# Optimization experiments

Measured on AMD Instinct MI355X. Metric: run time of the kernel, lower is better.

The kernel has to match this reference:

```python
import jax, jax.numpy as jnp
import numpy as np
from functools import partial

EPS = 1e-6
SINKHORN_ITERS = 10

def sinkhorn(logits):
    # log-space Sinkhorn normalization -> doubly-stochastic soft permutation
    M = logits
    for _ in range(SINKHORN_ITERS):
        M = M - jax.scipy.special.logsumexp(M, axis=1, keepdims=True)
        M = M - jax.scipy.special.logsumexp(M, axis=0, keepdims=True)
    return jnp.exp(M)

def r_poly(a):
    delta = 0.5 - a
    num = 0.25 + 1.65811 * delta + 2.15388 * delta**2 + 8.2844 * delta**3 + 6.16764 * delta**4
    den = a * (1.0 - a)
    den = jnp.where(jnp.abs(den) < EPS, EPS, den)
    return num / den

def power_r(x, y, ra, w0, w1):
    ra = jnp.where(jnp.abs(ra) < EPS, EPS, ra)
    return (w0 * x**ra + w1 * y**ra) ** (1.0 / ra)

def F_upper(x, y, a, w0, w1):
    # generalized combine for a in [0.5, 2); x,y pre-clamped to [EPS, 1-EPS]
    xy = x * y
    mn = jnp.minimum(x, y)
    lin = w0 * x + w1 * y
    p = jnp.sqrt(jnp.maximum(3.0 / jnp.maximum(2.0 - a, EPS) - 1.0, EPS))
    r1 = xy ** p                                      # 1.25 < a < 2
    r3 = 4.0 * ((1.25 - a) * mn + (a - 1.0) * xy)     # 1 < a < 1.25
    ra = r_poly(jnp.clip(a, 0.75, 1.0 - EPS))
    r5 = power_r(x, y, ra, w0, w1)                    # 0.75 <= a < 1
    R = r_poly(jnp.float32(0.75))
    r6 = (3.0 - 4.0 * a) * lin + (4.0 * a - 2.0) * power_r(x, y, R, w0, w1)
    r0 = jnp.where((jnp.abs(x - 1.0) < EPS) & (jnp.abs(y - 1.0) < EPS), 1.0, 0.0)
    out = lin                                          # a ~ 0.5 / fallback
    out = jnp.where((a > 0.5) & (a < 0.75), r6, out)
    out = jnp.where((a >= 0.75) & (a < 1.0), r5, out)
    out = jnp.where(jnp.abs(a - 1.0) < EPS, mn, out)
    out = jnp.where((a > 1.0) & (a < 1.25), r3, out)
    out = jnp.where(jnp.abs(a - 1.25) < EPS, xy, out)
    out = jnp.where((a > 1.25) & (a < 2.0), r1, out)
    out = jnp.where(jnp.abs(a - 2.0) < EPS, r0, out)
    return out

def F_comb(x, y, a, w0, w1):
    x = jnp.clip(jnp.nan_to_num(x, nan=EPS), EPS, 1.0 - EPS)
    y = jnp.clip(jnp.nan_to_num(y, nan=EPS), EPS, 1.0 - EPS)
    a = jnp.clip(jnp.nan_to_num(a, nan=-1.0, posinf=2.0 - EPS, neginf=-1.0 + EPS), -1.0 + EPS, 2.0 - EPS)
    hi = F_upper(x, y, a, w0, w1)
    a_flip = jnp.clip(1.0 - a, -1.0 + EPS, 2.0 - EPS)
    lo = 1.0 - F_upper(1.0 - x, 1.0 - y, a_flip, w0, w1)  # rule 8 (single-level recursion)
    return jnp.where(a < 0.5 - EPS, lo, hi)

def combine(left, right, w, b):
    w_soft = jax.nn.softmax(w)
    a_scaled = jax.nn.sigmoid(b) * 3.0 - 1.0
    nres = F_comb(left, right, a_scaled, w_soft[0], w_soft[1])
    return jnp.where(jnp.isnan(nres), a_scaled, nres)

def setup_inputs() -> dict:
    key = jax.random.key(0)
    k1, k2, k3, k4 = jax.random.split(key, 4)
    B, L = 65536, 256
    x = jax.random.uniform(k1, (B, L), dtype=jnp.float32)
    logits = jax.random.normal(k2, (L, L), dtype=jnp.float32)
    weights = jax.random.uniform(k3, (L - 1, 2), dtype=jnp.float32) + 0.5   # uniform(0.5, 1.5)
    biases = jax.random.uniform(k4, (L - 1,), dtype=jnp.float32) * 3.0 - 1.0
    return {"x": x, "logits": logits, "weights": weights, "biases": biases}

def reference(x, logits, weights, biases):
    P = sinkhorn(logits)                  # (L, L) soft permutation
    leaf_values = x @ P                   # (B, L)
    leaves = leaf_values.T                # (L, B)
    out0 = combine(leaves[0], leaves[1], weights[0], biases[0])

    def step(carry, inp):
        leaf, w, b = inp
        out = combine(carry, leaf, w, b)
        return out, None

    final, _ = jax.lax.scan(step, out0, (leaves[2:], weights[1:], biases[1:]))
    return final[:, None]                 # (B, 1)
```

## Files before the change

kernel.cpp:

```cpp
#include <hip/hip_runtime.h>

#define EPS 1e-6f

typedef unsigned short u16;
typedef u16   u16x4  __attribute__((ext_vector_type(4)));
typedef u16   u16x8  __attribute__((ext_vector_type(8)));
typedef float f32x4  __attribute__((ext_vector_type(4)));
typedef _Float16 f16x8 __attribute__((ext_vector_type(8)));

enum { BR_LIN = 0, BR_R6, BR_R5, BR_MIN, BR_R3, BR_XY, BR_R1, BR_R0 };

__device__ __forceinline__ u16 f2h(float f) { return __builtin_bit_cast(u16, (_Float16)f); }

__device__ __forceinline__ f16x8 lds_f16x8(const u16* p) {
  u16x8 r = *(const u16x8*)p;
  return __builtin_bit_cast(f16x8, r);
}

__device__ __forceinline__ f32x4 mfma16(f16x8 a, f16x8 b, f32x4 c) {
  return __builtin_amdgcn_mfma_f32_16x16x32_f16(a, b, c, 0, 0, 0);
}

__device__ __forceinline__ float fexp2(float x) {
  float r; asm("v_exp_f32 %0, %1" : "=v"(r) : "v"(x)); return r;
}
__device__ __forceinline__ float flog2(float x) {
  float r; asm("v_log_f32 %0, %1" : "=v"(r) : "v"(x)); return r;
}

__device__ __forceinline__ float r_poly_f(float a) {
  float d  = 0.5f - a;
  float d2 = d * d;
  float num = 0.25f + 1.65811f * d + 2.15388f * d2 + 8.2844f * d2 * d + 6.16764f * d2 * d2;
  float den = a * (1.0f - a);
  if (fabsf(den) < EPS) den = EPS;
  return num / den;
}

__device__ __forceinline__ void leaf_pre(float leaf, f32x4 p0, f32x4 p2,
                                         float& Y, float& w1Y, float& w1ey, float& cply) {
  float fx = p0[0], w1 = p0[2], rs = p2[0], cp = p2[2], sx = p2[3];
  float yy = fminf(fmaxf(leaf, EPS), 1.0f - EPS);
  Y = fmaf(sx, yy, fx);
  float ly = flog2(Y);
  w1Y  = w1 * Y;
  w1ey = w1 * fexp2(rs * ly);
  cply = cp * ly;
}

__device__ __forceinline__ float step_carry(float carry, float Y, float w1Y, float w1ey, float cply,
                                            f32x4 p0, f32x4 p1, f32x4 p2) {
  float fx = p0[0], w0 = p0[1], s_lin = p0[3];
  float s_mn = p1[0], s_xy = p1[1], s_pm = p1[2], s_pow = p1[3];
  float rs = p2[0], rinv = p2[1], cp = p2[2], sx = p2[3];

  float xx = fminf(fmaxf(carry, EPS), 1.0f - EPS);
  float X  = fmaf(sx, xx, fx);
  float lx = flog2(X);
  float pw = fexp2(fmaf(cp, lx, cply));
  float ex = fexp2(rs * lx);
  float s  = fmaf(w0, ex, w1ey);
  float pm = fexp2(rinv * flog2(s));

  float r = s_lin * fmaf(w0, X, w1Y);
  r = fmaf(s_mn, fminf(X, Y), r);
  r = fmaf(s_xy, X * Y, r);
  r = fmaf(s_pm, pm, r);
  r = fmaf(s_pow, pw, r);
  return fmaf(sx, r, fx);
}

__global__ __launch_bounds__(1024, 4) void sinkhorn_kernel(
    const float* __restrict__ logits, u16* __restrict__ PTf,
    const float* __restrict__ W, const float* __restrict__ Bv,
    float* __restrict__ prm12) {
  const int t  = threadIdx.x;

  if (t < 255) {
    int i = t;
    float w0r = W[2 * i], w1r = W[2 * i + 1];
    float m  = fmaxf(w0r, w1r);
    float e0 = expf(w0r - m), e1 = expf(w1r - m);
    float inv = 1.0f / (e0 + e1);
    float w0 = e0 * inv, w1 = e1 * inv;

    float b   = Bv[i];
    float sig = 1.0f / (1.0f + expf(-b));
    float a_fb = sig * 3.0f - 1.0f;

    float a = a_fb;
    if (__builtin_isnan(a)) a = -1.0f;
    a = fminf(fmaxf(a, -1.0f + EPS), 2.0f - EPS);
    int flip = (a < 0.5f - EPS) ? 1 : 0;
    float aa = a;
    if (flip) aa = fminf(fmaxf(1.0f - a, -1.0f + EPS), 2.0f - EPS);

    int br; float c0 = 0.f, c1 = 0.f, c2 = 0.f, c3 = 0.f;
    if (fabsf(aa - 2.0f) < EPS) br = BR_R0;
    else if (aa > 1.25f && aa < 2.0f) {
      br = BR_R1;
      c0 = sqrtf(fmaxf(3.0f / fmaxf(2.0f - aa, EPS) - 1.0f, EPS));
    } else if (fabsf(aa - 1.25f) < EPS) br = BR_XY;
    else if (aa > 1.0f && aa < 1.25f) { br = BR_R3; c0 = 1.25f - aa; c1 = aa - 1.0f; }
    else if (fabsf(aa - 1.0f) < EPS) br = BR_MIN;
    else if (aa >= 0.75f && aa < 1.0f) {
      br = BR_R5;
      float ac = fminf(fmaxf(aa, 0.75f), 1.0f - EPS);
      float ra = r_poly_f(ac);
      if (fabsf(ra) < EPS) ra = EPS;
      c0 = ra; c1 = 1.0f / ra;
    } else if (aa > 0.5f && aa < 0.75f) {
      br = BR_R6;
      c0 = 3.0f - 4.0f * aa; c1 = 4.0f * aa - 2.0f;
      float R = r_poly_f(0.75f);
      if (fabsf(R) < EPS) R = EPS;
      c2 = R; c3 = 1.0f / R;
    } else br = BR_LIN;

    float s_lin = 0.f, s_mn = 0.f, s_xy = 0.f, s_pm = 0.f, s_pow = 0.f;
    float rs = 1.0f, rinv = 1.0f, cp = 0.0f;
    if (br == BR_R1)       { s_pow = 1.0f; cp = c0; }
    else if (br == BR_XY)  { s_xy = 1.0f; }
    else if (br == BR_R3)  { s_mn = 4.0f * c0; s_xy = 4.0f * c1; }
    else if (br == BR_MIN) { s_mn = 1.0f; }
    else if (br == BR_R5)  { s_pm = 1.0f; rs = c0; rinv = c1; }
    else if (br == BR_R6)  { s_lin = c0; s_pm = c1; rs = c2; rinv = c3; }
    else if (br == BR_LIN) { s_lin = 1.0f; }

    float* o12 = prm12 + i * 12;
    o12[0] = (float)flip; o12[1] = w0;  o12[2] = w1;   o12[3] = s_lin;
    o12[4] = s_mn;        o12[5] = s_xy; o12[6] = s_pm; o12[7] = s_pow;
    o12[8] = rs;          o12[9] = rinv; o12[10] = cp;  o12[11] = 1.0f - 2.0f * (float)flip;
  }

  __shared__ float alpha[256], beta[256];
  __shared__ float psum[256][33];

  const int R  = t >> 5;
  const int C  = t & 31;
  const int r0 = R << 3;

  float e[8][8];
  #pragma unroll
  for (int dr = 0; dr < 8; ++dr) {
    const float* row = logits + (r0 + dr) * 256 + C;
    #pragma unroll
    for (int m = 0; m < 8; ++m) e[dr][m] = __expf(row[m << 5]);
  }

  if (t < 256) beta[t] = 1.0f;
  __syncthreads();

  for (int it = 0; it < 10; ++it) {
    {
      float bv[8], acc[8];
      #pragma unroll
      for (int m = 0; m < 8; ++m) bv[m] = beta[C + (m << 5)];
      #pragma unroll
      for (int dr = 0; dr < 8; ++dr) {
        float s = 0.f;
        #pragma unroll
        for (int m = 0; m < 8; ++m) s += e[dr][m] * bv[m];
        acc[dr] = s;
      }
      #pragma unroll
      for (int dr = 0; dr < 8; ++dr) psum[r0 + dr][C] = acc[dr];
    }
    __syncthreads();
    if (t < 256) {
      float s = 0.f;
      #pragma unroll
      for (int j = 0; j < 32; ++j) s += psum[t][j];
      alpha[t] = 1.0f / s;
    }
    __syncthreads();
    {
      float av[8], acc[8];
      #pragma unroll
      for (int dr = 0; dr < 8; ++dr) av[dr] = alpha[r0 + dr];
      #pragma unroll
      for (int m = 0; m < 8; ++m) {
        float s = 0.f;
        #pragma unroll
        for (int dr = 0; dr < 8; ++dr) s += e[dr][m] * av[dr];
        acc[m] = s;
      }
      #pragma unroll
      for (int m = 0; m < 8; ++m) psum[C + (m << 5)][R] = acc[m];
    }
    __syncthreads();
    if (t < 256) {
      float s = 0.f;
      #pragma unroll
      for (int j = 0; j < 32; ++j) s += psum[t][j];
      beta[t] = 1.0f / s;
    }
    __syncthreads();
  }

  float av[8], bv[8];
  #pragma unroll
  for (int dr = 0; dr < 8; ++dr) av[dr] = alpha[r0 + dr];
  #pragma unroll
  for (int m = 0; m < 8; ++m) bv[m] = beta[C + (m << 5)];

  #pragma unroll
  for (int m = 0; m < 8; ++m) {
    int l = C + (m << 5);
    u16x8 vh;
    #pragma unroll
    for (int dr = 0; dr < 8; ++dr) vh[dr] = f2h(av[dr] * e[dr][m] * bv[m]);
    *(u16x8*)(PTf + l * 256 + r0) = vh;
  }
}

#define CSTR 68

__global__ __launch_bounds__(256, 4) void gemm_chain_kernel(
    const float* __restrict__ x, const u16* __restrict__ PTf,
    const float* __restrict__ prm12, float* __restrict__ out) {
  __shared__ __align__(16) char smem[32768];
  u16* xs = (u16*)smem;
  u16* pt = (u16*)(smem + 4096);
  float* qlds = (float*)(smem + 20480);
  float* cbuf = (float*)smem;

  const int t    = threadIdx.x;
  const int w    = t >> 6;
  const int lane = t & 63;
  const int bl   = lane & 15;
  const int kh   = lane >> 4;
  const int wm   = w >> 1;
  const int wn   = w & 1;
  const int b0   = blockIdx.x * 64;

  const int xrow = t >> 2;
  const int xsl  = t & 3;

  for (int j = t; j < 3060; j += 256) qlds[j] = prm12[j];

  f32x4 acc[8][2];
  #pragma unroll
  for (int m = 0; m < 8; ++m) {
    acc[m][0] = f32x4{0.f, 0.f, 0.f, 0.f};
    acc[m][1] = f32x4{0.f, 0.f, 0.f, 0.f};
  }

  f32x4 xr[2];
  u16x8 pr[4];

  #pragma unroll
  for (int j = 0; j < 2; ++j)
    xr[j] = *(const f32x4*)(x + (b0 + xrow) * 256 + ((xsl + 4 * j) << 2));
  #pragma unroll
  for (int j = 0; j < 4; ++j) {
    int c = t + 256 * j, r = c >> 2, s = c & 3, g = s ^ ((r >> 1) & 3);
    pr[j] = *(const u16x8*)(PTf + r * 256 + (g << 3));
  }

  for (int kc = 0; kc < 8; ++kc) {
    #pragma unroll
    for (int j = 0; j < 2; ++j) {
      int slot = xsl + 4 * j;
      u16x4 hv;
      #pragma unroll
      for (int e = 0; e < 4; ++e) hv[e] = f2h(xr[j][e]);
      int g = slot >> 1, sub = slot & 1;
      *(u16x4*)(xs + xrow * 32 + ((g ^ ((xrow >> 1) & 3)) << 3) + (sub << 2)) = hv;
    }
    #pragma unroll
    for (int j = 0; j < 4; ++j)
      *(u16x8*)(pt + ((t + 256 * j) << 3)) = pr[j];
    __syncthreads();

    if (kc < 7) {
      int k1 = (kc + 1) << 5;
      #pragma unroll
      for (int j = 0; j < 2; ++j)
        xr[j] = *(const f32x4*)(x + (b0 + xrow) * 256 + k1 + ((xsl + 4 * j) << 2));
      #pragma unroll
      for (int j = 0; j < 4; ++j) {
        int c = t + 256 * j, r = c >> 2, s = c & 3, g = s ^ ((r >> 1) & 3);
        pr[j] = *(const u16x8*)(PTf + r * 256 + k1 + (g << 3));
      }
    }

    f16x8 bh[2];
    #pragma unroll
    for (int nf = 0; nf < 2; ++nf) {
      int brow = (wn << 5) + (nf << 4) + bl;
      bh[nf] = lds_f16x8(xs + brow * 32 + ((kh ^ ((brow >> 1) & 3)) << 3));
    }
    #pragma unroll
    for (int mf = 0; mf < 8; ++mf) {
      int arow = (wm << 7) + (mf << 4) + bl;
      f16x8 ah = lds_f16x8(pt + arow * 32 + ((kh ^ ((arow >> 1) & 3)) << 3));
      #pragma unroll
      for (int nf = 0; nf < 2; ++nf)
        acc[mf][nf] = mfma16(ah, bh[nf], acc[mf][nf]);
    }
    __syncthreads();
  }

  float carry = 0.0f;

  #pragma unroll
  for (int c = 0; c < 4; ++c) {
    __syncthreads();
    if (wm == (c >> 1)) {
      #pragma unroll
      for (int d = 0; d < 4; ++d) {
        int mf = ((c & 1) << 2) + d;
        #pragma unroll
        for (int nf = 0; nf < 2; ++nf) {
          int bc = (wn << 5) + (nf << 4) + bl;
          #pragma unroll
          for (int r = 0; r < 4; ++r) {
            int lr = (d << 4) + (kh << 2) + r;
            cbuf[lr * CSTR + bc] = acc[mf][nf][r];
          }
        }
      }
    }
    __syncthreads();
    if (t < 64) {
      int lc0 = 0;
      if (c == 0) {
        float v0 = cbuf[0 * CSTR + t];
        float v1 = cbuf[1 * CSTR + t];
        float v2 = cbuf[2 * CSTR + t];
        float v3 = cbuf[3 * CSTR + t];
        carry = v0;
        float vv[3] = {v1, v2, v3};
        #pragma unroll
        for (int u = 0; u < 3; ++u) {
          const float* qn = qlds + u * 12;
          f32x4 P0 = *(const f32x4*)(qn), P1 = *(const f32x4*)(qn + 4), P2 = *(const f32x4*)(qn + 8);
          float Y, w1Y, w1ey, cply;
          leaf_pre(vv[u], P0, P2, Y, w1Y, w1ey, cply);
          carry = step_carry(carry, Y, w1Y, w1ey, cply, P0, P1, P2);
        }
        lc0 = 4;
      }
      for (int lc = lc0; lc < 64; lc += 4) {
        float v[4];
        #pragma unroll
        for (int u = 0; u < 4; ++u) v[u] = cbuf[(lc + u) * CSTR + t];
        f32x4 P0[4], P1[4], P2[4];
        #pragma unroll
        for (int u = 0; u < 4; ++u) {
          const float* qn = qlds + ((c << 6) + lc + u - 1) * 12;
          P0[u] = *(const f32x4*)(qn);
          P1[u] = *(const f32x4*)(qn + 4);
          P2[u] = *(const f32x4*)(qn + 8);
        }
        float Y[4], w1Y[4], w1ey[4], cply[4];
        #pragma unroll
        for (int u = 0; u < 4; ++u)
          leaf_pre(v[u], P0[u], P2[u], Y[u], w1Y[u], w1ey[u], cply[u]);
        #pragma unroll
        for (int u = 0; u < 4; ++u)
          carry = step_carry(carry, Y[u], w1Y[u], w1ey[u], cply[u], P0[u], P1[u], P2[u]);
      }
    }
  }
  if (t < 64) out[b0 + t] = carry;
}

extern "C" void kernel_launch(void* const* d_in, const int* in_sizes, int n_in,
                              void* d_out, int out_size, void* d_ws, size_t ws_size,
                              hipStream_t stream) {
  const float* x       = (const float*)d_in[0];
  const float* logits  = (const float*)d_in[1];
  const float* weights = (const float*)d_in[2];
  const float* biases  = (const float*)d_in[3];
  float* out = (float*)d_out;

  char* ws = (char*)d_ws;
  int Btot = in_sizes[0] / 256;

  u16*   PTf   = (u16*)ws;
  float* prm12 = (float*)(ws + 131072);

  sinkhorn_kernel<<<1, 1024, 0, stream>>>(logits, PTf, weights, biases, prm12);
  gemm_chain_kernel<<<Btot / 64, 256, 0, stream>>>(x, PTf, prm12, out);
}
```

Baseline: 70.26 us.

## Load GEMM operands straight from global into MFMA registers, dropping LDS staging

The GEMM main loop no longer stages x and the permutation matrix through shared memory with barriers. Each lane now loads its MFMA fragments directly from global memory: x as fp32, converted in registers, and P^T as fp16 read per fragment, with x double-buffered in registers. This removes the LDS writes and reads and the two __syncthreads per k-chunk, and shrinks the shared allocation. In exchange, P^T fragments are fetched redundantly from global/L2 by every wave, and the per-lane strided loads are less coalesced.

```diff
diff --git a/kernel.cpp b/kernel.cpp
--- a/kernel.cpp
+++ b/kernel.cpp
@@ -3,7 +3,6 @@
 #define EPS 1e-6f
 
 typedef unsigned short u16;
-typedef u16   u16x4  __attribute__((ext_vector_type(4)));
 typedef u16   u16x8  __attribute__((ext_vector_type(8)));
 typedef float f32x4  __attribute__((ext_vector_type(4)));
 typedef _Float16 f16x8 __attribute__((ext_vector_type(8)));
@@ -12,13 +11,17 @@
 
 __device__ __forceinline__ u16 f2h(float f) { return __builtin_bit_cast(u16, (_Float16)f); }
 
-__device__ __forceinline__ f16x8 lds_f16x8(const u16* p) {
-  u16x8 r = *(const u16x8*)p;
-  return __builtin_bit_cast(f16x8, r);
-}
-
 __device__ __forceinline__ f32x4 mfma16(f16x8 a, f16x8 b, f32x4 c) {
   return __builtin_amdgcn_mfma_f32_16x16x32_f16(a, b, c, 0, 0, 0);
+}
+
+__device__ __forceinline__ f16x8 cvt8(f32x4 lo, f32x4 hi) {
+  f16x8 r;
+  r[0] = (_Float16)lo[0]; r[1] = (_Float16)lo[1];
+  r[2] = (_Float16)lo[2]; r[3] = (_Float16)lo[3];
+  r[4] = (_Float16)hi[0]; r[5] = (_Float16)hi[1];
+  r[6] = (_Float16)hi[2]; r[7] = (_Float16)hi[3];
+  return r;
 }
 
 __device__ __forceinline__ float fexp2(float x) {
@@ -216,14 +219,33 @@
 
 #define CSTR 68
 
+#define GEMM_BODY(KC, BCUR, BNXT)                                              \
+  {                                                                            \
+    f16x8 bh0 = cvt8(BCUR[0], BCUR[1]);                                        \
+    f16x8 bh1 = cvt8(BCUR[2], BCUR[3]);                                        \
+    if ((KC) < 7) {                                                            \
+      int kn = ((KC) + 1) << 5;                                                \
+      BNXT[0] = *(const f32x4*)(xb0 + kn);                                     \
+      BNXT[1] = *(const f32x4*)(xb0 + kn + 4);                                 \
+      BNXT[2] = *(const f32x4*)(xb1 + kn);                                     \
+      BNXT[3] = *(const f32x4*)(xb1 + kn + 4);                                 \
+    }                                                                          \
+    int ka = ((KC) << 5) + k0;                                                 \
+    _Pragma("unroll")                                                          \
+    for (int mf = 0; mf < 8; ++mf) {                                           \
+      u16x8 avr = *(const u16x8*)(pa + mf * 4096 + ka);                        \
+      f16x8 ah  = __builtin_bit_cast(f16x8, avr);                              \
+      acc[mf][0] = mfma16(ah, bh0, acc[mf][0]);                                \
+      acc[mf][1] = mfma16(ah, bh1, acc[mf][1]);                                \
+    }                                                                          \
+  }
+
 __global__ __launch_bounds__(256, 4) void gemm_chain_kernel(
     const float* __restrict__ x, const u16* __restrict__ PTf,
     const float* __restrict__ prm12, float* __restrict__ out) {
-  __shared__ __align__(16) char smem[32768];
-  u16* xs = (u16*)smem;
-  u16* pt = (u16*)(smem + 4096);
-  float* qlds = (float*)(smem + 20480);
+  __shared__ __align__(16) char smem[30720];
   float* cbuf = (float*)smem;
+  float* qlds = (float*)(smem + 17408);
 
   const int t    = threadIdx.x;
   const int w    = t >> 6;
@@ -234,9 +256,6 @@
   const int wn   = w & 1;
   const int b0   = blockIdx.x * 64;
 
-  const int xrow = t >> 2;
-  const int xsl  = t & 3;
-
   for (int j = t; j < 3060; j += 256) qlds[j] = prm12[j];
 
   f32x4 acc[8][2];
@@ -246,61 +265,25 @@
     acc[m][1] = f32x4{0.f, 0.f, 0.f, 0.f};
   }
 
-  f32x4 xr[2];
-  u16x8 pr[4];
-
-  #pragma unroll
-  for (int j = 0; j < 2; ++j)
-    xr[j] = *(const f32x4*)(x + (b0 + xrow) * 256 + ((xsl + 4 * j) << 2));
-  #pragma unroll
-  for (int j = 0; j < 4; ++j) {
-    int c = t + 256 * j, r = c >> 2, s = c & 3, g = s ^ ((r >> 1) & 3);
-    pr[j] = *(const u16x8*)(PTf + r * 256 + (g << 3));
-  }
-
-  for (int kc = 0; kc < 8; ++kc) {
-    #pragma unroll
-    for (int j = 0; j < 2; ++j) {
-      int slot = xsl + 4 * j;
-      u16x4 hv;
-      #pragma unroll
-      for (int e = 0; e < 4; ++e) hv[e] = f2h(xr[j][e]);
-      int g = slot >> 1, sub = slot & 1;
-      *(u16x4*)(xs + xrow * 32 + ((g ^ ((xrow >> 1) & 3)) << 3) + (sub << 2)) = hv;
-    }
-    #pragma unroll
-    for (int j = 0; j < 4; ++j)
-      *(u16x8*)(pt + ((t + 256 * j) << 3)) = pr[j];
-    __syncthreads();
-
-    if (kc < 7) {
-      int k1 = (kc + 1) << 5;
-      #pragma unroll
-      for (int j = 0; j < 2; ++j)
-        xr[j] = *(const f32x4*)(x + (b0 + xrow) * 256 + k1 + ((xsl + 4 * j) << 2));
-      #pragma unroll
-      for (int j = 0; j < 4; ++j) {
-        int c = t + 256 * j, r = c >> 2, s = c & 3, g = s ^ ((r >> 1) & 3);
-        pr[j] = *(const u16x8*)(PTf + r * 256 + k1 + (g << 3));
-      }
-    }
-
-    f16x8 bh[2];
-    #pragma unroll
-    for (int nf = 0; nf < 2; ++nf) {
-      int brow = (wn << 5) + (nf << 4) + bl;
-      bh[nf] = lds_f16x8(xs + brow * 32 + ((kh ^ ((brow >> 1) & 3)) << 3));
-    }
-    #pragma unroll
-    for (int mf = 0; mf < 8; ++mf) {
-      int arow = (wm << 7) + (mf << 4) + bl;
-      f16x8 ah = lds_f16x8(pt + arow * 32 + ((kh ^ ((arow >> 1) & 3)) << 3));
-      #pragma unroll
-      for (int nf = 0; nf < 2; ++nf)
-        acc[mf][nf] = mfma16(ah, bh[nf], acc[mf][nf]);
-    }
-    __syncthreads();
-  }
+  const float* xb0 = x + (size_t)(b0 + (wn << 5) + bl) * 256 + (kh << 3);
+  const float* xb1 = xb0 + 16 * 256;
+  const u16*   pa  = PTf + ((wm << 7) + bl) * 256;
+  const int    k0  = kh << 3;
+
+  f32x4 bxA[4], bxB[4];
+  bxA[0] = *(const f32x4*)(xb0);
+  bxA[1] = *(const f32x4*)(xb0 + 4);
+  bxA[2] = *(const f32x4*)(xb1);
+  bxA[3] = *(const f32x4*)(xb1 + 4);
+
+  GEMM_BODY(0, bxA, bxB)
+  GEMM_BODY(1, bxB, bxA)
+  GEMM_BODY(2, bxA, bxB)
+  GEMM_BODY(3, bxB, bxA)
+  GEMM_BODY(4, bxA, bxB)
+  GEMM_BODY(5, bxB, bxA)
+  GEMM_BODY(6, bxA, bxB)
+  GEMM_BODY(7, bxB, bxA)
 
   float carry = 0.0f;
 
```

New measurement: 98.96 us. 40.9% more time.
